# Optimization experiments

Measured on AMD Instinct MI355X. Metric: run time of the kernel, lower is better.

The kernel has to match this reference:

```python
import jax, jax.numpy as jnp
import numpy as np
import math

B, S, DIM = 2, 2048, 2048
H, KV, HD = 16, 1, 128  # query heads, kv heads, head dim


def setup_inputs() -> dict:
    key = jax.random.key(0)
    ks = jax.random.split(key, 6)
    std = 0.02
    return {
        "hidden_states": jax.random.normal(ks[0], (B, S, DIM), jnp.float32),
        "attention_mask": jnp.zeros((B, 1, S, S), jnp.float32),
        "wq": jax.random.normal(ks[1], (DIM, H * HD), jnp.float32) * std,
        "bq": jnp.zeros((H * HD,), jnp.float32),
        "wk": jax.random.normal(ks[2], (DIM, KV * HD), jnp.float32) * std,
        "bk": jnp.zeros((KV * HD,), jnp.float32),
        "wv": jax.random.normal(ks[3], (DIM, KV * HD), jnp.float32) * std,
        "bv": jnp.zeros((KV * HD,), jnp.float32),
        "wo": jax.random.normal(ks[4], (H * HD, DIM), jnp.float32) * std,
        "bo": jnp.zeros((DIM,), jnp.float32),
    }


def reference(hidden_states, attention_mask, wq, bq, wk, bk, wv, bv, wo, bo):
    b, s, _ = hidden_states.shape
    q = (hidden_states @ wq + bq).reshape(b, s, H, HD)
    k = (hidden_states @ wk + bk).reshape(b, s, KV, HD)
    v = (hidden_states @ wv + bv).reshape(b, s, KV, HD)
    # [b, h, s, d]
    q = jnp.transpose(q, (0, 2, 1, 3))
    k = jnp.transpose(k, (0, 2, 1, 3))
    v = jnp.transpose(v, (0, 2, 1, 3))
    # broadcast shared KV heads to all query heads (num_kv_heads < num_query_heads)
    repeats = H // KV
    k = jnp.repeat(k, repeats, axis=1)
    v = jnp.repeat(v, repeats, axis=1)
    scores = jnp.einsum('bhqd,bhkd->bhqk', q, k) / math.sqrt(HD)
    scores = scores + attention_mask
    weights = jax.nn.softmax(scores, axis=-1)
    attn = jnp.einsum('bhqk,bhkd->bhqd', weights, v)
    attn = jnp.transpose(attn, (0, 2, 1, 3)).reshape(b, s, H * HD)
    return attn @ wo + bo
```

## Files before the change

kernel.cpp:

```cpp
#include <hip/hip_runtime.h>
#include <hip/hip_bf16.h>
#include <stdint.h>

#define S_LEN 2048
#define DIMSZ 2048
#define NH    16
#define HD    128
#define NQK   2176
#define NQKV  2304

typedef short  bf16x8  __attribute__((ext_vector_type(8)));
typedef float  floatx4 __attribute__((ext_vector_type(4)));
typedef float  floatx16 __attribute__((ext_vector_type(16)));
typedef int    intx4   __attribute__((ext_vector_type(4)));
typedef unsigned short u16;

#define mfma32 __builtin_amdgcn_mfma_f32_32x32x16_bf16
#define LOG2E 1.4426950408889634f

__device__ __forceinline__ u16 f2bf(float x) {
  unsigned int u = __builtin_bit_cast(unsigned int, x);
  u = (u + 0x7FFFu + ((u >> 16) & 1u)) >> 16;
  return (u16)u;
}

__device__ __forceinline__ int cvtpk(float lo, float hi) {
  int r;
  asm("v_cvt_pk_bf16_f32 %0, %1, %2" : "=v"(r) : "v"(lo), "v"(hi));
  return r;
}

#if __has_builtin(__builtin_amdgcn_exp2f)
__device__ __forceinline__ float fexp2(float x) { return __builtin_amdgcn_exp2f(x); }
#else
__device__ __forceinline__ float fexp2(float x) { return exp2f(x); }
#endif

#if __has_builtin(__builtin_amdgcn_permlane32_swap)
__device__ __forceinline__ void half_swap(int& a, int& b) {
  auto r = __builtin_amdgcn_permlane32_swap(a, b, false, false);
  a = (int)r[0]; b = (int)r[1];
}
__device__ __forceinline__ float red_max32(float x) {
  int xi = __builtin_bit_cast(int, x);
  auto r = __builtin_amdgcn_permlane32_swap(xi, xi, false, false);
  return fmaxf(__builtin_bit_cast(float, (int)r[0]), __builtin_bit_cast(float, (int)r[1]));
}
__device__ __forceinline__ float red_add32(float x) {
  int xi = __builtin_bit_cast(int, x);
  auto r = __builtin_amdgcn_permlane32_swap(xi, xi, false, false);
  return __builtin_bit_cast(float, (int)r[0]) + __builtin_bit_cast(float, (int)r[1]);
}
#else
__device__ __forceinline__ void half_swap(int& a, int& b) {
  int as = __shfl_xor(a, 32);
  int bs = __shfl_xor(b, 32);
  int lane = threadIdx.x & 63;
  int na = (lane < 32) ? a : bs;
  int nb = (lane < 32) ? as : b;
  a = na; b = nb;
}
__device__ __forceinline__ float red_max32(float x) { return fmaxf(x, __shfl_xor(x, 32)); }
__device__ __forceinline__ float red_add32(float x) { return x + __shfl_xor(x, 32); }
#endif

__device__ __forceinline__ void gload16(const void* g, void* l) {
  __builtin_amdgcn_global_load_lds(
      reinterpret_cast<const __attribute__((address_space(1))) void*>(reinterpret_cast<uintptr_t>(g)),
      reinterpret_cast<__attribute__((address_space(3))) void*>(reinterpret_cast<uintptr_t>(l)),
      16, 0, 0);
}

__global__ void k_cvt_bf16(const float* __restrict__ in, u16* __restrict__ out, int n4) {
  int i = blockIdx.x * blockDim.x + threadIdx.x;
  if (i < n4) {
    float4 v = ((const float4*)in)[i];
    ushort4 o;
    o.x = f2bf(v.x); o.y = f2bf(v.y); o.z = f2bf(v.z); o.w = f2bf(v.w);
    ((ushort4*)out)[i] = o;
  }
}

__global__ void k_transpose_bf16(const float* __restrict__ in, u16* __restrict__ out,
                                 int K, int N, int rowOff) {
  __shared__ float t[64][65];
  int c0 = blockIdx.x * 64;
  int r0 = blockIdx.y * 64;
  int tid = threadIdx.x;
  int lr = tid >> 6;
  int lc = tid & 63;
#pragma unroll
  for (int i = 0; i < 16; ++i) {
    int r = lr + i * 4;
    t[r][lc] = in[(size_t)(r0 + r) * N + c0 + lc];
  }
  __syncthreads();
#pragma unroll
  for (int i = 0; i < 16; ++i) {
    int r = lr + i * 4;
    out[(size_t)(rowOff + c0 + r) * K + r0 + lc] = f2bf(t[lc][r]);
  }
}

__global__ void k_bias_concat(const float* __restrict__ bq, const float* __restrict__ bk,
                              const float* __restrict__ bv, float* __restrict__ out) {
  int i = blockIdx.x * 256 + threadIdx.x;
  if (i < NQKV) out[i] = (i < 2048) ? bq[i] : (i < NQK ? bk[i - 2048] : bv[i - NQK]);
}

__device__ __forceinline__ void stage_tile(const u16* __restrict__ G, int ldg, int row0, int kt,
                                           u16* lbase, int wid, int lane) {
#pragma unroll
  for (int i = 0; i < 4; ++i) {
    int c   = (wid * 4 + i) * 64 + lane;
    int row = c >> 3, cin = c & 7;
    int cs  = cin ^ (row & 7);
    const u16* g = G + (size_t)(row0 + row) * ldg + kt * 64 + cs * 8;
    gload16(g, (char*)lbase + (wid * 4 + i) * 1024);
  }
}

template <int OMODE>
__global__ __launch_bounds__(256)
void k_gemm(const u16* __restrict__ A, const u16* __restrict__ Bt,
            const float* __restrict__ bias, void* __restrict__ Cout,
            u16* __restrict__ vt, int M, int N, int K) {
  __shared__ u16 lA[2][128 * 64];
  __shared__ u16 lB[2][128 * 64];
  const int tid = threadIdx.x, lane = tid & 63, wid = tid >> 6;
  const int wm = wid >> 1, wn = wid & 1;
  const int tm = blockIdx.x, tn = blockIdx.y;
  const int nk = K >> 6;

  stage_tile(A, K, tm * 128, 0, lA[0], wid, lane);
  stage_tile(Bt, K, tn * 128, 0, lB[0], wid, lane);
  __syncthreads();

  floatx4 acc[4][4] = {};
  int buf = 0;
  for (int kt = 0; kt < nk; ++kt) {
    if (kt + 1 < nk) {
      stage_tile(A, K, tm * 128, kt + 1, lA[buf ^ 1], wid, lane);
      stage_tile(Bt, K, tn * 128, kt + 1, lB[buf ^ 1], wid, lane);
    }
    const char* pa = (const char*)&lA[buf][0];
    const char* pb = (const char*)&lB[buf][0];
#pragma unroll
    for (int kk = 0; kk < 2; ++kk) {
      bf16x8 af[4], bfr[4];
      int gch = kk * 4 + (lane >> 4);
#pragma unroll
      for (int f = 0; f < 4; ++f) {
        int ra = wm * 64 + f * 16 + (lane & 15);
        af[f]  = *(const bf16x8*)(pa + ra * 128 + ((gch ^ (ra & 7)) << 4));
        int rb = wn * 64 + f * 16 + (lane & 15);
        bfr[f] = *(const bf16x8*)(pb + rb * 128 + ((gch ^ (rb & 7)) << 4));
      }
      __builtin_amdgcn_s_setprio(1);
#pragma unroll
      for (int fm = 0; fm < 4; ++fm)
#pragma unroll
        for (int fn = 0; fn < 4; ++fn)
          acc[fm][fn] = __builtin_amdgcn_mfma_f32_16x16x32_bf16(af[fm], bfr[fn], acc[fm][fn], 0, 0, 0);
      __builtin_amdgcn_s_setprio(0);
    }
    __syncthreads();
    buf ^= 1;
  }

#pragma unroll
  for (int fm = 0; fm < 4; ++fm)
#pragma unroll
    for (int fn = 0; fn < 4; ++fn)
#pragma unroll
      for (int r = 0; r < 4; ++r) {
        int rowg = tm * 128 + wm * 64 + fm * 16 + (lane >> 4) * 4 + r;
        int colg = tn * 128 + wn * 64 + fn * 16 + (lane & 15);
        float v = acc[fm][fn][r] + bias[colg];
        if constexpr (OMODE == 1) {
          ((float*)Cout)[(size_t)rowg * N + colg] = v;
        } else {
          if (colg < NQK) {
            ((u16*)Cout)[(size_t)rowg * N + colg] = f2bf(v);
          } else {
            int d = colg - NQK;
            int bg = rowg >> 11, s = rowg & 2047;
            vt[((size_t)bg * HD + d) * S_LEN + s] = f2bf(v);
          }
        }
      }
}

__device__ __forceinline__ void stage_kv(const u16* __restrict__ qkv, const u16* __restrict__ vt,
                                         int b, int kt, u16* lK, u16* lV, int wid, int lane) {
#pragma unroll
  for (int i = 0; i < 2; ++i) {
    int seg = wid * 2 + i;
    {
      int r = seg * 4 + (lane >> 4), cin = lane & 15;
      const u16* g = qkv + (size_t)(b * S_LEN + kt * 64 + r) * NQKV + 2048 + ((cin ^ (r & 7)) * 8);
      gload16(g, (char*)lK + seg * 1024);
    }
    {
      int r = seg * 8 + (lane >> 3), cin = lane & 7;
      const u16* g = vt + ((size_t)b * HD + r) * S_LEN + kt * 64 + ((cin ^ (r & 7)) * 8);
      gload16(g, (char*)lV + seg * 1024);
    }
  }
}

__global__ __launch_bounds__(512)
void k_attn(const u16* __restrict__ qkv, const u16* __restrict__ vt,
            const float* __restrict__ mask, u16* __restrict__ attn) {
  __shared__ __align__(16) u16   lK[2][64 * 128];
  __shared__ __align__(16) u16   lV[2][128 * 64];
  __shared__ __align__(16) float lM[2][32 * 64];
  const int tid = threadIdx.x, lane = tid & 63, wid = tid >> 6;
  const int qt = blockIdx.x, hg = blockIdx.y, b = blockIdx.z;
  const int h = hg * 8 + wid;
  const int q = lane & 31, h5 = lane >> 5;
  const float c_sl2 = 0.08838834764831845f * LOG2E;

  bf16x8 qf[8];
  const size_t qrow = (size_t)(b * S_LEN + qt * 32 + q);
#pragma unroll
  for (int cs = 0; cs < 8; ++cs)
    qf[cs] = *(const bf16x8*)(qkv + qrow * NQKV + h * HD + cs * 16 + h5 * 8);

  float m_ = -1e30f, l_ = 0.f;
  floatx16 acco[4] = {};

  const int mq = tid >> 4, mc = tid & 15;
  const float* mrow = mask + (size_t)b * S_LEN * S_LEN + (size_t)(qt * 32 + mq) * S_LEN + mc * 4;

  stage_kv(qkv, vt, b, 0, lK[0], lV[0], wid, lane);
  floatx4 mreg = *(const floatx4*)(mrow);
  *(floatx4*)((char*)&lM[0][0] + mq * 256 + ((mc ^ (mq & 7)) << 4)) = mreg * LOG2E;
  __syncthreads();

  int buf = 0;
  for (int kt = 0; kt < S_LEN / 64; ++kt) {
    if (kt + 1 < S_LEN / 64) {
      stage_kv(qkv, vt, b, kt + 1, lK[buf ^ 1], lV[buf ^ 1], wid, lane);
      mreg = *(const floatx4*)(mrow + (size_t)(kt + 1) * 64);
    }

    floatx16 accs0 = {}, accs1 = {};
    const char* pK = (const char*)&lK[buf][0];
    __builtin_amdgcn_s_setprio(1);
#pragma unroll
    for (int cs = 0; cs < 8; ++cs) {
      int c = cs * 2 + h5;
      bf16x8 kf0 = *(const bf16x8*)(pK + q * 256 + ((c ^ (q & 7)) << 4));
      bf16x8 kf1 = *(const bf16x8*)(pK + (32 + q) * 256 + ((c ^ (q & 7)) << 4));
      accs0 = mfma32(kf0, qf[cs], accs0, 0, 0, 0);
      accs1 = mfma32(kf1, qf[cs], accs1, 0, 0, 0);
    }
    __builtin_amdgcn_s_setprio(0);

    float pr[32];
    float rowm = -1e30f;
    const char* pM = (const char*)&lM[buf][0];
#pragma unroll
    for (int kb = 0; kb < 2; ++kb)
#pragma unroll
      for (int rg = 0; rg < 4; ++rg) {
        int c = kb * 8 + rg * 2 + h5;
        floatx4 m4 = *(const floatx4*)(pM + q * 256 + ((c ^ (q & 7)) << 4));
#pragma unroll
        for (int t = 0; t < 4; ++t) {
          float sv = (kb ? accs1[rg * 4 + t] : accs0[rg * 4 + t]) * c_sl2 + m4[t];
          pr[kb * 16 + rg * 4 + t] = sv;
          rowm = fmaxf(rowm, sv);
        }
      }
    rowm = red_max32(rowm);
    if (__any(rowm > m_ + 11.5415603f)) {
      float mn = fmaxf(m_, rowm);
      float al = fexp2(m_ - mn);
      m_ = mn;
      l_ *= al;
#pragma unroll
      for (int dt = 0; dt < 4; ++dt) acco[dt] *= al;
    }
    float sum = 0.f;
#pragma unroll
    for (int j = 0; j < 32; ++j) {
      float e = fexp2(pr[j] - m_);
      pr[j] = e;
      sum += e;
    }
    l_ += red_add32(sum);

    bf16x8 pf[4];
#pragma unroll
    for (int kb = 0; kb < 2; ++kb)
#pragma unroll
      for (int s = 0; s < 2; ++s) {
        int base = kb * 16 + s * 8;
        int A0 = cvtpk(pr[base + 0], pr[base + 1]);
        int A1 = cvtpk(pr[base + 2], pr[base + 3]);
        int B0 = cvtpk(pr[base + 4], pr[base + 5]);
        int B1 = cvtpk(pr[base + 6], pr[base + 7]);
        half_swap(A0, B0);
        half_swap(A1, B1);
        intx4 w;
        w[0] = A0; w[1] = A1; w[2] = B0; w[3] = B1;
        pf[kb * 2 + s] = __builtin_bit_cast(bf16x8, w);
      }

    const char* pV = (const char*)&lV[buf][0];
    __builtin_amdgcn_s_setprio(1);
#pragma unroll
    for (int dt = 0; dt < 4; ++dt) {
      int rd = dt * 32 + q;
#pragma unroll
      for (int ks = 0; ks < 4; ++ks) {
        int c = ks * 2 + h5;
        bf16x8 vf = *(const bf16x8*)(pV + rd * 128 + ((c ^ (q & 7)) << 4));
        acco[dt] = mfma32(vf, pf[ks], acco[dt], 0, 0, 0);
      }
    }
    __builtin_amdgcn_s_setprio(0);

    if (kt + 1 < S_LEN / 64)
      *(floatx4*)((char*)&lM[buf ^ 1][0] + mq * 256 + ((mc ^ (mq & 7)) << 4)) = mreg * LOG2E;
    __syncthreads();
    buf ^= 1;
  }

  float inv = 1.0f / l_;
  u16* obase = attn + qrow * DIMSZ + h * HD;
#pragma unroll
  for (int dt = 0; dt < 4; ++dt)
#pragma unroll
    for (int rg = 0; rg < 4; ++rg) {
      int d0 = dt * 32 + rg * 8 + h5 * 4;
      ushort4 st;
      st.x = f2bf(acco[dt][rg * 4 + 0] * inv);
      st.y = f2bf(acco[dt][rg * 4 + 1] * inv);
      st.z = f2bf(acco[dt][rg * 4 + 2] * inv);
      st.w = f2bf(acco[dt][rg * 4 + 3] * inv);
      *(ushort4*)(obase + d0) = st;
    }
}

extern "C" void kernel_launch(void* const* d_in, const int* in_sizes, int n_in,
                              void* d_out, int out_size, void* d_ws, size_t ws_size,
                              hipStream_t stream) {
  const float* hidden = (const float*)d_in[0];
  const float* mask   = (const float*)d_in[1];
  const float* wq = (const float*)d_in[2];
  const float* bq = (const float*)d_in[3];
  const float* wk = (const float*)d_in[4];
  const float* bk = (const float*)d_in[5];
  const float* wv = (const float*)d_in[6];
  const float* bv = (const float*)d_in[7];
  const float* wo = (const float*)d_in[8];
  const float* bo = (const float*)d_in[9];
  float* out = (float*)d_out;

  char* ws = (char*)d_ws;
  u16*   hb    = (u16*)(ws);
  u16*   wqkvT = (u16*)(ws + 16777216);
  u16*   woT   = (u16*)(ws + 26214400);
  float* bqkv  = (float*)(ws + 34603008);
  u16*   qkv   = (u16*)(ws + 34612224);
  u16*   vt    = (u16*)(ws + 53486592);
  u16*   attn  = (u16*)(ws + 54535168);

  k_cvt_bf16<<<dim3(8192), dim3(256), 0, stream>>>(hidden, hb, 4096 * 2048 / 4);
  k_transpose_bf16<<<dim3(32, 32), dim3(256), 0, stream>>>(wq, wqkvT, 2048, 2048, 0);
  k_transpose_bf16<<<dim3(2, 32),  dim3(256), 0, stream>>>(wk, wqkvT, 2048, 128, 2048);
  k_transpose_bf16<<<dim3(2, 32),  dim3(256), 0, stream>>>(wv, wqkvT, 2048, 128, NQK);
  k_transpose_bf16<<<dim3(32, 32), dim3(256), 0, stream>>>(wo, woT, 2048, 2048, 0);
  k_bias_concat<<<dim3(9), dim3(256), 0, stream>>>(bq, bk, bv, bqkv);

  k_gemm<0><<<dim3(32, 18), dim3(256), 0, stream>>>(hb, wqkvT, bqkv, (void*)qkv, vt, 4096, NQKV, 2048);
  k_attn<<<dim3(64, 2, 2), dim3(512), 0, stream>>>(qkv, vt, mask, attn);
  k_gemm<1><<<dim3(32, 16), dim3(256), 0, stream>>>(attn, woT, bo, (void*)out, (u16*)nullptr, 4096, 2048, 2048);
}
```

Before: 204.7 us.

## Software-pipeline the P·V MFMA of the previous tile with the current softmax

The attention loop now runs the P·V MFMAs for the previous key tile split around the exp/sum phase of the current tile, so matrix-core work overlaps the VALU softmax. V staging is split from K staging and shifted one iteration later, and the P fragments are carried across iterations, with a final P·V epilogue after the loop. Row-max and row-sum reductions use four independent accumulators to shorten dependency chains. This holds extra live registers (pf_prev) and reorders the rescale, which may raise register pressure and lower occupancy.

```diff
diff --git a/kernel.cpp b/kernel.cpp
--- a/kernel.cpp
+++ b/kernel.cpp
@@ -8,6 +8,7 @@
 #define HD    128
 #define NQK   2176
 #define NQKV  2304
+#define NT    (S_LEN / 64)
 
 typedef short  bf16x8  __attribute__((ext_vector_type(8)));
 typedef float  floatx4 __attribute__((ext_vector_type(4)));
@@ -191,21 +192,24 @@
       }
 }
 
-__device__ __forceinline__ void stage_kv(const u16* __restrict__ qkv, const u16* __restrict__ vt,
-                                         int b, int kt, u16* lK, u16* lV, int wid, int lane) {
+__device__ __forceinline__ void stage_k(const u16* __restrict__ qkv, int b, int kt,
+                                        u16* lK, int wid, int lane) {
 #pragma unroll
   for (int i = 0; i < 2; ++i) {
     int seg = wid * 2 + i;
-    {
-      int r = seg * 4 + (lane >> 4), cin = lane & 15;
-      const u16* g = qkv + (size_t)(b * S_LEN + kt * 64 + r) * NQKV + 2048 + ((cin ^ (r & 7)) * 8);
-      gload16(g, (char*)lK + seg * 1024);
-    }
-    {
-      int r = seg * 8 + (lane >> 3), cin = lane & 7;
-      const u16* g = vt + ((size_t)b * HD + r) * S_LEN + kt * 64 + ((cin ^ (r & 7)) * 8);
-      gload16(g, (char*)lV + seg * 1024);
-    }
+    int r = seg * 4 + (lane >> 4), cin = lane & 15;
+    const u16* g = qkv + (size_t)(b * S_LEN + kt * 64 + r) * NQKV + 2048 + ((cin ^ (r & 7)) * 8);
+    gload16(g, (char*)lK + seg * 1024);
+  }
+}
+__device__ __forceinline__ void stage_v(const u16* __restrict__ vt, int b, int kt,
+                                        u16* lV, int wid, int lane) {
+#pragma unroll
+  for (int i = 0; i < 2; ++i) {
+    int seg = wid * 2 + i;
+    int r = seg * 8 + (lane >> 3), cin = lane & 7;
+    const u16* g = vt + ((size_t)b * HD + r) * S_LEN + kt * 64 + ((cin ^ (r & 7)) * 8);
+    gload16(g, (char*)lV + seg * 1024);
   }
 }
 
@@ -229,21 +233,23 @@
 
   float m_ = -1e30f, l_ = 0.f;
   floatx16 acco[4] = {};
+  bf16x8 pf_prev[4];
 
   const int mq = tid >> 4, mc = tid & 15;
   const float* mrow = mask + (size_t)b * S_LEN * S_LEN + (size_t)(qt * 32 + mq) * S_LEN + mc * 4;
 
-  stage_kv(qkv, vt, b, 0, lK[0], lV[0], wid, lane);
+  stage_k(qkv, b, 0, lK[0], wid, lane);
   floatx4 mreg = *(const floatx4*)(mrow);
   *(floatx4*)((char*)&lM[0][0] + mq * 256 + ((mc ^ (mq & 7)) << 4)) = mreg * LOG2E;
   __syncthreads();
 
   int buf = 0;
-  for (int kt = 0; kt < S_LEN / 64; ++kt) {
-    if (kt + 1 < S_LEN / 64) {
-      stage_kv(qkv, vt, b, kt + 1, lK[buf ^ 1], lV[buf ^ 1], wid, lane);
+  for (int kt = 0; kt < NT; ++kt) {
+    if (kt + 1 < NT) {
+      stage_k(qkv, b, kt + 1, lK[buf ^ 1], wid, lane);
       mreg = *(const floatx4*)(mrow + (size_t)(kt + 1) * 64);
     }
+    stage_v(vt, b, kt, lV[buf], wid, lane);
 
     floatx16 accs0 = {}, accs1 = {};
     const char* pK = (const char*)&lK[buf][0];
@@ -259,7 +265,7 @@
     __builtin_amdgcn_s_setprio(0);
 
     float pr[32];
-    float rowm = -1e30f;
+    float pm0 = -1e30f, pm1 = -1e30f, pm2 = -1e30f, pm3 = -1e30f;
     const char* pM = (const char*)&lM[buf][0];
 #pragma unroll
     for (int kb = 0; kb < 2; ++kb)
@@ -267,32 +273,71 @@
       for (int rg = 0; rg < 4; ++rg) {
         int c = kb * 8 + rg * 2 + h5;
         floatx4 m4 = *(const floatx4*)(pM + q * 256 + ((c ^ (q & 7)) << 4));
-#pragma unroll
-        for (int t = 0; t < 4; ++t) {
-          float sv = (kb ? accs1[rg * 4 + t] : accs0[rg * 4 + t]) * c_sl2 + m4[t];
-          pr[kb * 16 + rg * 4 + t] = sv;
-          rowm = fmaxf(rowm, sv);
-        }
-      }
-    rowm = red_max32(rowm);
-    if (__any(rowm > m_ + 11.5415603f)) {
+        float s0 = (kb ? accs1[rg * 4 + 0] : accs0[rg * 4 + 0]) * c_sl2 + m4[0];
+        float s1 = (kb ? accs1[rg * 4 + 1] : accs0[rg * 4 + 1]) * c_sl2 + m4[1];
+        float s2 = (kb ? accs1[rg * 4 + 2] : accs0[rg * 4 + 2]) * c_sl2 + m4[2];
+        float s3 = (kb ? accs1[rg * 4 + 3] : accs0[rg * 4 + 3]) * c_sl2 + m4[3];
+        pr[kb * 16 + rg * 4 + 0] = s0; pm0 = fmaxf(pm0, s0);
+        pr[kb * 16 + rg * 4 + 1] = s1; pm1 = fmaxf(pm1, s1);
+        pr[kb * 16 + rg * 4 + 2] = s2; pm2 = fmaxf(pm2, s2);
+        pr[kb * 16 + rg * 4 + 3] = s3; pm3 = fmaxf(pm3, s3);
+      }
+    float rowm = red_max32(fmaxf(fmaxf(pm0, pm1), fmaxf(pm2, pm3)));
+
+    bool need = __any(rowm > m_ + 11.5415603f);
+    float al = 1.0f;
+    if (need) {
       float mn = fmaxf(m_, rowm);
-      float al = fexp2(m_ - mn);
+      al = fexp2(m_ - mn);
       m_ = mn;
       l_ *= al;
+    }
+
+    const char* pV = (const char*)&lV[buf ^ 1][0];
+    if (kt > 0) {
+      __builtin_amdgcn_s_setprio(1);
+#pragma unroll
+      for (int dt = 0; dt < 2; ++dt) {
+        int rd = dt * 32 + q;
+#pragma unroll
+        for (int ks = 0; ks < 4; ++ks) {
+          int c = ks * 2 + h5;
+          bf16x8 vf = *(const bf16x8*)(pV + rd * 128 + ((c ^ (q & 7)) << 4));
+          acco[dt] = mfma32(vf, pf_prev[ks], acco[dt], 0, 0, 0);
+        }
+      }
+      __builtin_amdgcn_s_setprio(0);
+    }
+
+    float ps0 = 0.f, ps1 = 0.f, ps2 = 0.f, ps3 = 0.f;
+#pragma unroll
+    for (int j = 0; j < 32; j += 4) {
+      float e0 = fexp2(pr[j + 0] - m_); pr[j + 0] = e0; ps0 += e0;
+      float e1 = fexp2(pr[j + 1] - m_); pr[j + 1] = e1; ps1 += e1;
+      float e2 = fexp2(pr[j + 2] - m_); pr[j + 2] = e2; ps2 += e2;
+      float e3 = fexp2(pr[j + 3] - m_); pr[j + 3] = e3; ps3 += e3;
+    }
+    l_ += red_add32((ps0 + ps1) + (ps2 + ps3));
+
+    if (kt > 0) {
+      __builtin_amdgcn_s_setprio(1);
+#pragma unroll
+      for (int dt = 2; dt < 4; ++dt) {
+        int rd = dt * 32 + q;
+#pragma unroll
+        for (int ks = 0; ks < 4; ++ks) {
+          int c = ks * 2 + h5;
+          bf16x8 vf = *(const bf16x8*)(pV + rd * 128 + ((c ^ (q & 7)) << 4));
+          acco[dt] = mfma32(vf, pf_prev[ks], acco[dt], 0, 0, 0);
+        }
+      }
+      __builtin_amdgcn_s_setprio(0);
+    }
+    if (need) {
 #pragma unroll
       for (int dt = 0; dt < 4; ++dt) acco[dt] *= al;
     }
-    float sum = 0.f;
-#pragma unroll
-    for (int j = 0; j < 32; ++j) {
-      float e = fexp2(pr[j] - m_);
-      pr[j] = e;
-      sum += e;
-    }
-    l_ += red_add32(sum);
-
-    bf16x8 pf[4];
+
 #pragma unroll
     for (int kb = 0; kb < 2; ++kb)
 #pragma unroll
@@ -306,10 +351,17 @@
         half_swap(A1, B1);
         intx4 w;
         w[0] = A0; w[1] = A1; w[2] = B0; w[3] = B1;
-        pf[kb * 2 + s] = __builtin_bit_cast(bf16x8, w);
-      }
-
-    const char* pV = (const char*)&lV[buf][0];
+        pf_prev[kb * 2 + s] = __builtin_bit_cast(bf16x8, w);
+      }
+
+    if (kt + 1 < NT)
+      *(floatx4*)((char*)&lM[buf ^ 1][0] + mq * 256 + ((mc ^ (mq & 7)) << 4)) = mreg * LOG2E;
+    __syncthreads();
+    buf ^= 1;
+  }
+
+  {
+    const char* pV = (const char*)&lV[buf ^ 1][0];
     __builtin_amdgcn_s_setprio(1);
 #pragma unroll
     for (int dt = 0; dt < 4; ++dt) {
@@ -318,15 +370,10 @@
       for (int ks = 0; ks < 4; ++ks) {
         int c = ks * 2 + h5;
         bf16x8 vf = *(const bf16x8*)(pV + rd * 128 + ((c ^ (q & 7)) << 4));
-        acco[dt] = mfma32(vf, pf[ks], acco[dt], 0, 0, 0);
+        acco[dt] = mfma32(vf, pf_prev[ks], acco[dt], 0, 0, 0);
       }
     }
     __builtin_amdgcn_s_setprio(0);
-
-    if (kt + 1 < S_LEN / 64)
-      *(floatx4*)((char*)&lM[buf ^ 1][0] + mq * 256 + ((mc ^ (mq & 7)) << 4)) = mreg * LOG2E;
-    __syncthreads();
-    buf ^= 1;
   }
 
   float inv = 1.0f / l_;
```

New measurement: 207.1 us. No clear change (+1.1%).

## Halve GEMM K-tile to cut LDS and raise occupancy; split softmax reductions

Applied to the files above, without the earlier changes.

The projection GEMM now stages 128x32 K-slices instead of 128x64, halving shared memory per block. It uses a matching 4-chunk XOR swizzle and asks for three blocks per CU through launch bounds, so more waves can overlap memory latency. In the attention kernel the row max and row sum are split into four independent accumulators to shorten the serial dependency chains. The cost is twice as many K iterations and barriers in the GEMM, with less compute per sync.

```diff
diff --git a/kernel.cpp b/kernel.cpp
--- a/kernel.cpp
+++ b/kernel.cpp
@@ -8,6 +8,7 @@
 #define HD    128
 #define NQK   2176
 #define NQKV  2304
+#define NT    (S_LEN / 64)
 
 typedef short  bf16x8  __attribute__((ext_vector_type(8)));
 typedef float  floatx4 __attribute__((ext_vector_type(4)));
@@ -108,62 +109,59 @@
   if (i < NQKV) out[i] = (i < 2048) ? bq[i] : (i < NQK ? bk[i - 2048] : bv[i - NQK]);
 }
 
-__device__ __forceinline__ void stage_tile(const u16* __restrict__ G, int ldg, int row0, int kt,
-                                           u16* lbase, int wid, int lane) {
-#pragma unroll
-  for (int i = 0; i < 4; ++i) {
-    int c   = (wid * 4 + i) * 64 + lane;
-    int row = c >> 3, cin = c & 7;
-    int cs  = cin ^ (row & 7);
-    const u16* g = G + (size_t)(row0 + row) * ldg + kt * 64 + cs * 8;
-    gload16(g, (char*)lbase + (wid * 4 + i) * 1024);
+__device__ __forceinline__ void stage_tile32(const u16* __restrict__ G, int ldg, int row0, int kt,
+                                             u16* lbase, int wid, int lane) {
+#pragma unroll
+  for (int i = 0; i < 2; ++i) {
+    int c   = (wid * 2 + i) * 64 + lane;
+    int row = c >> 2, cin = c & 3;
+    int cs  = cin ^ ((row >> 1) & 3);
+    const u16* g = G + (size_t)(row0 + row) * ldg + kt * 32 + cs * 8;
+    gload16(g, (char*)lbase + (wid * 2 + i) * 1024);
   }
 }
 
 template <int OMODE>
-__global__ __launch_bounds__(256)
+__global__ __launch_bounds__(256, 3)
 void k_gemm(const u16* __restrict__ A, const u16* __restrict__ Bt,
             const float* __restrict__ bias, void* __restrict__ Cout,
             u16* __restrict__ vt, int M, int N, int K) {
-  __shared__ u16 lA[2][128 * 64];
-  __shared__ u16 lB[2][128 * 64];
+  __shared__ u16 lA[2][128 * 32];
+  __shared__ u16 lB[2][128 * 32];
   const int tid = threadIdx.x, lane = tid & 63, wid = tid >> 6;
   const int wm = wid >> 1, wn = wid & 1;
   const int tm = blockIdx.x, tn = blockIdx.y;
-  const int nk = K >> 6;
-
-  stage_tile(A, K, tm * 128, 0, lA[0], wid, lane);
-  stage_tile(Bt, K, tn * 128, 0, lB[0], wid, lane);
+  const int nk = K >> 5;
+  const int g3 = lane >> 4;
+
+  stage_tile32(A, K, tm * 128, 0, lA[0], wid, lane);
+  stage_tile32(Bt, K, tn * 128, 0, lB[0], wid, lane);
   __syncthreads();
 
   floatx4 acc[4][4] = {};
   int buf = 0;
   for (int kt = 0; kt < nk; ++kt) {
     if (kt + 1 < nk) {
-      stage_tile(A, K, tm * 128, kt + 1, lA[buf ^ 1], wid, lane);
-      stage_tile(Bt, K, tn * 128, kt + 1, lB[buf ^ 1], wid, lane);
+      stage_tile32(A, K, tm * 128, kt + 1, lA[buf ^ 1], wid, lane);
+      stage_tile32(Bt, K, tn * 128, kt + 1, lB[buf ^ 1], wid, lane);
     }
     const char* pa = (const char*)&lA[buf][0];
     const char* pb = (const char*)&lB[buf][0];
-#pragma unroll
-    for (int kk = 0; kk < 2; ++kk) {
-      bf16x8 af[4], bfr[4];
-      int gch = kk * 4 + (lane >> 4);
-#pragma unroll
-      for (int f = 0; f < 4; ++f) {
-        int ra = wm * 64 + f * 16 + (lane & 15);
-        af[f]  = *(const bf16x8*)(pa + ra * 128 + ((gch ^ (ra & 7)) << 4));
-        int rb = wn * 64 + f * 16 + (lane & 15);
-        bfr[f] = *(const bf16x8*)(pb + rb * 128 + ((gch ^ (rb & 7)) << 4));
-      }
-      __builtin_amdgcn_s_setprio(1);
-#pragma unroll
-      for (int fm = 0; fm < 4; ++fm)
-#pragma unroll
-        for (int fn = 0; fn < 4; ++fn)
-          acc[fm][fn] = __builtin_amdgcn_mfma_f32_16x16x32_bf16(af[fm], bfr[fn], acc[fm][fn], 0, 0, 0);
-      __builtin_amdgcn_s_setprio(0);
-    }
+    bf16x8 af[4], bfr[4];
+#pragma unroll
+    for (int f = 0; f < 4; ++f) {
+      int ra = wm * 64 + f * 16 + (lane & 15);
+      af[f]  = *(const bf16x8*)(pa + ra * 64 + ((g3 ^ ((ra >> 1) & 3)) << 4));
+      int rb = wn * 64 + f * 16 + (lane & 15);
+      bfr[f] = *(const bf16x8*)(pb + rb * 64 + ((g3 ^ ((rb >> 1) & 3)) << 4));
+    }
+    __builtin_amdgcn_s_setprio(1);
+#pragma unroll
+    for (int fm = 0; fm < 4; ++fm)
+#pragma unroll
+      for (int fn = 0; fn < 4; ++fn)
+        acc[fm][fn] = __builtin_amdgcn_mfma_f32_16x16x32_bf16(af[fm], bfr[fn], acc[fm][fn], 0, 0, 0);
+    __builtin_amdgcn_s_setprio(0);
     __syncthreads();
     buf ^= 1;
   }
@@ -239,8 +237,8 @@
   __syncthreads();
 
   int buf = 0;
-  for (int kt = 0; kt < S_LEN / 64; ++kt) {
-    if (kt + 1 < S_LEN / 64) {
+  for (int kt = 0; kt < NT; ++kt) {
+    if (kt + 1 < NT) {
       stage_kv(qkv, vt, b, kt + 1, lK[buf ^ 1], lV[buf ^ 1], wid, lane);
       mreg = *(const floatx4*)(mrow + (size_t)(kt + 1) * 64);
     }
@@ -259,7 +257,7 @@
     __builtin_amdgcn_s_setprio(0);
 
     float pr[32];
-    float rowm = -1e30f;
+    float pm0 = -1e30f, pm1 = -1e30f, pm2 = -1e30f, pm3 = -1e30f;
     const char* pM = (const char*)&lM[buf][0];
 #pragma unroll
     for (int kb = 0; kb < 2; ++kb)
@@ -267,14 +265,17 @@
       for (int rg = 0; rg < 4; ++rg) {
         int c = kb * 8 + rg * 2 + h5;
         floatx4 m4 = *(const floatx4*)(pM + q * 256 + ((c ^ (q & 7)) << 4));
-#pragma unroll
-        for (int t = 0; t < 4; ++t) {
-          float sv = (kb ? accs1[rg * 4 + t] : accs0[rg * 4 + t]) * c_sl2 + m4[t];
-          pr[kb * 16 + rg * 4 + t] = sv;
-          rowm = fmaxf(rowm, sv);
-        }
+        float s0 = (kb ? accs1[rg * 4 + 0] : accs0[rg * 4 + 0]) * c_sl2 + m4[0];
+        float s1 = (kb ? accs1[rg * 4 + 1] : accs0[rg * 4 + 1]) * c_sl2 + m4[1];
+        float s2 = (kb ? accs1[rg * 4 + 2] : accs0[rg * 4 + 2]) * c_sl2 + m4[2];
+        float s3 = (kb ? accs1[rg * 4 + 3] : accs0[rg * 4 + 3]) * c_sl2 + m4[3];
+        pr[kb * 16 + rg * 4 + 0] = s0; pm0 = fmaxf(pm0, s0);
+        pr[kb * 16 + rg * 4 + 1] = s1; pm1 = fmaxf(pm1, s1);
+        pr[kb * 16 + rg * 4 + 2] = s2; pm2 = fmaxf(pm2, s2);
+        pr[kb * 16 + rg * 4 + 3] = s3; pm3 = fmaxf(pm3, s3);
       }
-    rowm = red_max32(rowm);
+    float rowm = red_max32(fmaxf(fmaxf(pm0, pm1), fmaxf(pm2, pm3)));
+
     if (__any(rowm > m_ + 11.5415603f)) {
       float mn = fmaxf(m_, rowm);
       float al = fexp2(m_ - mn);
@@ -283,14 +284,15 @@
 #pragma unroll
       for (int dt = 0; dt < 4; ++dt) acco[dt] *= al;
     }
-    float sum = 0.f;
-#pragma unroll
-    for (int j = 0; j < 32; ++j) {
-      float e = fexp2(pr[j] - m_);
-      pr[j] = e;
-      sum += e;
-    }
-    l_ += red_add32(sum);
+    float ps0 = 0.f, ps1 = 0.f, ps2 = 0.f, ps3 = 0.f;
+#pragma unroll
+    for (int j = 0; j < 32; j += 4) {
+      float e0 = fexp2(pr[j + 0] - m_); pr[j + 0] = e0; ps0 += e0;
+      float e1 = fexp2(pr[j + 1] - m_); pr[j + 1] = e1; ps1 += e1;
+      float e2 = fexp2(pr[j + 2] - m_); pr[j + 2] = e2; ps2 += e2;
+      float e3 = fexp2(pr[j + 3] - m_); pr[j + 3] = e3; ps3 += e3;
+    }
+    l_ += red_add32((ps0 + ps1) + (ps2 + ps3));
 
     bf16x8 pf[4];
 #pragma unroll
@@ -323,7 +325,7 @@
     }
     __builtin_amdgcn_s_setprio(0);
 
-    if (kt + 1 < S_LEN / 64)
+    if (kt + 1 < NT)
       *(floatx4*)((char*)&lM[buf ^ 1][0] + mq * 256 + ((mc ^ (mq & 7)) << 4)) = mreg * LOG2E;
     __syncthreads();
     buf ^= 1;
```

Result: no change. 204.2 us (-0.3%).

## Use partial vmcnt waits and async mask staging to deepen load pipelining

Applied to the files above, without the earlier changes.

Replaces the full __syncthreads in the GEMM and attention loops with explicit s_waitcnt vmcnt(N) plus raw barriers, so the next tile's global-to-LDS loads stay in flight while the current tile is computed. The attention mask is now loaded straight into LDS through the same direct-load path instead of going through registers, and the log2e scaling moves into the exp argument. Max and sum reductions are split into four independent accumulators to shorten dependency chains, and the rescale threshold changes. The hand-counted vmcnt values must match the exact number of issued loads, or the kernel reads stale LDS.

```diff
diff --git a/kernel.cpp b/kernel.cpp
--- a/kernel.cpp
+++ b/kernel.cpp
@@ -8,6 +8,7 @@
 #define HD    128
 #define NQK   2176
 #define NQKV  2304
+#define NT    (S_LEN / 64)
 
 typedef short  bf16x8  __attribute__((ext_vector_type(8)));
 typedef float  floatx4 __attribute__((ext_vector_type(4)));
@@ -134,7 +135,6 @@
 
   stage_tile(A, K, tm * 128, 0, lA[0], wid, lane);
   stage_tile(Bt, K, tn * 128, 0, lB[0], wid, lane);
-  __syncthreads();
 
   floatx4 acc[4][4] = {};
   int buf = 0;
@@ -142,7 +142,11 @@
     if (kt + 1 < nk) {
       stage_tile(A, K, tm * 128, kt + 1, lA[buf ^ 1], wid, lane);
       stage_tile(Bt, K, tn * 128, kt + 1, lB[buf ^ 1], wid, lane);
-    }
+      asm volatile("s_waitcnt vmcnt(8)" ::: "memory");
+    } else {
+      asm volatile("s_waitcnt vmcnt(0)" ::: "memory");
+    }
+    __builtin_amdgcn_s_barrier();
     const char* pa = (const char*)&lA[buf][0];
     const char* pb = (const char*)&lB[buf][0];
 #pragma unroll
@@ -164,7 +168,7 @@
           acc[fm][fn] = __builtin_amdgcn_mfma_f32_16x16x32_bf16(af[fm], bfr[fn], acc[fm][fn], 0, 0, 0);
       __builtin_amdgcn_s_setprio(0);
     }
-    __syncthreads();
+    __builtin_amdgcn_s_barrier();
     buf ^= 1;
   }
 
@@ -191,8 +195,9 @@
       }
 }
 
-__device__ __forceinline__ void stage_kv(const u16* __restrict__ qkv, const u16* __restrict__ vt,
-                                         int b, int kt, u16* lK, u16* lV, int wid, int lane) {
+__device__ __forceinline__ void stage_kvm(const u16* __restrict__ qkv, const u16* __restrict__ vt,
+                                          const float* __restrict__ mask, int b, int qt, int kt,
+                                          u16* lK, u16* lV, float* lM, int wid, int lane) {
 #pragma unroll
   for (int i = 0; i < 2; ++i) {
     int seg = wid * 2 + i;
@@ -206,6 +211,12 @@
       const u16* g = vt + ((size_t)b * HD + r) * S_LEN + kt * 64 + ((cin ^ (r & 7)) * 8);
       gload16(g, (char*)lV + seg * 1024);
     }
+  }
+  {
+    int mq = wid * 4 + (lane >> 4), mc = lane & 15;
+    int cs = mc ^ (mq & 7);
+    const float* g = mask + ((size_t)b * S_LEN + qt * 32 + mq) * S_LEN + kt * 64 + cs * 4;
+    gload16(g, (char*)lM + wid * 1024);
   }
 }
 
@@ -219,7 +230,7 @@
   const int qt = blockIdx.x, hg = blockIdx.y, b = blockIdx.z;
   const int h = hg * 8 + wid;
   const int q = lane & 31, h5 = lane >> 5;
-  const float c_sl2 = 0.08838834764831845f * LOG2E;
+  const float scale = 0.08838834764831845f;
 
   bf16x8 qf[8];
   const size_t qrow = (size_t)(b * S_LEN + qt * 32 + q);
@@ -230,20 +241,17 @@
   float m_ = -1e30f, l_ = 0.f;
   floatx16 acco[4] = {};
 
-  const int mq = tid >> 4, mc = tid & 15;
-  const float* mrow = mask + (size_t)b * S_LEN * S_LEN + (size_t)(qt * 32 + mq) * S_LEN + mc * 4;
-
-  stage_kv(qkv, vt, b, 0, lK[0], lV[0], wid, lane);
-  floatx4 mreg = *(const floatx4*)(mrow);
-  *(floatx4*)((char*)&lM[0][0] + mq * 256 + ((mc ^ (mq & 7)) << 4)) = mreg * LOG2E;
-  __syncthreads();
+  stage_kvm(qkv, vt, mask, b, qt, 0, lK[0], lV[0], lM[0], wid, lane);
 
   int buf = 0;
-  for (int kt = 0; kt < S_LEN / 64; ++kt) {
-    if (kt + 1 < S_LEN / 64) {
-      stage_kv(qkv, vt, b, kt + 1, lK[buf ^ 1], lV[buf ^ 1], wid, lane);
-      mreg = *(const floatx4*)(mrow + (size_t)(kt + 1) * 64);
-    }
+  for (int kt = 0; kt < NT; ++kt) {
+    if (kt + 1 < NT) {
+      stage_kvm(qkv, vt, mask, b, qt, kt + 1, lK[buf ^ 1], lV[buf ^ 1], lM[buf ^ 1], wid, lane);
+      asm volatile("s_waitcnt vmcnt(5)" ::: "memory");
+    } else {
+      asm volatile("s_waitcnt vmcnt(0)" ::: "memory");
+    }
+    __builtin_amdgcn_s_barrier();
 
     floatx16 accs0 = {}, accs1 = {};
     const char* pK = (const char*)&lK[buf][0];
@@ -259,7 +267,7 @@
     __builtin_amdgcn_s_setprio(0);
 
     float pr[32];
-    float rowm = -1e30f;
+    float pm0 = -1e30f, pm1 = -1e30f, pm2 = -1e30f, pm3 = -1e30f;
     const char* pM = (const char*)&lM[buf][0];
 #pragma unroll
     for (int kb = 0; kb < 2; ++kb)
@@ -267,30 +275,35 @@
       for (int rg = 0; rg < 4; ++rg) {
         int c = kb * 8 + rg * 2 + h5;
         floatx4 m4 = *(const floatx4*)(pM + q * 256 + ((c ^ (q & 7)) << 4));
-#pragma unroll
-        for (int t = 0; t < 4; ++t) {
-          float sv = (kb ? accs1[rg * 4 + t] : accs0[rg * 4 + t]) * c_sl2 + m4[t];
-          pr[kb * 16 + rg * 4 + t] = sv;
-          rowm = fmaxf(rowm, sv);
-        }
-      }
-    rowm = red_max32(rowm);
-    if (__any(rowm > m_ + 11.5415603f)) {
+        float s0 = (kb ? accs1[rg * 4 + 0] : accs0[rg * 4 + 0]) * scale + m4[0];
+        float s1 = (kb ? accs1[rg * 4 + 1] : accs0[rg * 4 + 1]) * scale + m4[1];
+        float s2 = (kb ? accs1[rg * 4 + 2] : accs0[rg * 4 + 2]) * scale + m4[2];
+        float s3 = (kb ? accs1[rg * 4 + 3] : accs0[rg * 4 + 3]) * scale + m4[3];
+        pr[kb * 16 + rg * 4 + 0] = s0; pm0 = fmaxf(pm0, s0);
+        pr[kb * 16 + rg * 4 + 1] = s1; pm1 = fmaxf(pm1, s1);
+        pr[kb * 16 + rg * 4 + 2] = s2; pm2 = fmaxf(pm2, s2);
+        pr[kb * 16 + rg * 4 + 3] = s3; pm3 = fmaxf(pm3, s3);
+      }
+    float rowm = red_max32(fmaxf(fmaxf(pm0, pm1), fmaxf(pm2, pm3)));
+
+    if (__any(rowm > m_ + 8.0f)) {
       float mn = fmaxf(m_, rowm);
-      float al = fexp2(m_ - mn);
+      float al = fexp2((m_ - mn) * LOG2E);
       m_ = mn;
       l_ *= al;
 #pragma unroll
       for (int dt = 0; dt < 4; ++dt) acco[dt] *= al;
     }
-    float sum = 0.f;
-#pragma unroll
-    for (int j = 0; j < 32; ++j) {
-      float e = fexp2(pr[j] - m_);
-      pr[j] = e;
-      sum += e;
-    }
-    l_ += red_add32(sum);
+    float nml2 = -m_ * LOG2E;
+    float ps0 = 0.f, ps1 = 0.f, ps2 = 0.f, ps3 = 0.f;
+#pragma unroll
+    for (int j = 0; j < 32; j += 4) {
+      float e0 = fexp2(pr[j + 0] * LOG2E + nml2); pr[j + 0] = e0; ps0 += e0;
+      float e1 = fexp2(pr[j + 1] * LOG2E + nml2); pr[j + 1] = e1; ps1 += e1;
+      float e2 = fexp2(pr[j + 2] * LOG2E + nml2); pr[j + 2] = e2; ps2 += e2;
+      float e3 = fexp2(pr[j + 3] * LOG2E + nml2); pr[j + 3] = e3; ps3 += e3;
+    }
+    l_ += red_add32((ps0 + ps1) + (ps2 + ps3));
 
     bf16x8 pf[4];
 #pragma unroll
@@ -323,9 +336,7 @@
     }
     __builtin_amdgcn_s_setprio(0);
 
-    if (kt + 1 < S_LEN / 64)
-      *(floatx4*)((char*)&lM[buf ^ 1][0] + mq * 256 + ((mc ^ (mq & 7)) << 4)) = mreg * LOG2E;
-    __syncthreads();
+    __builtin_amdgcn_s_barrier();
     buf ^= 1;
   }
 
```

Result: no change. 207.0 us (+1.1%).
